# Kernel tuning notes

Measured on AMD Instinct MI355X. Metric: run time of the kernel, lower is better.

## Reference

```python
import jax, jax.numpy as jnp
import numpy as np
from functools import partial

SIGMA = 0.1       # blend_params.sigma (heaviside noise intensity)
GAMMA = 0.1       # blend_params.gamma (argmax noise intensity / z softening)
ZNEAR = 1.0
ZFAR = 100.0
NB_SAMPLES = 4
EPS = 1e-10
N, H, W, K = 8, 256, 256, 8


def random_heaviside(x, noise, sigma):
    # x: (N,H,W,K), noise: (S,N,H,W,K). torch.heaviside(v, ones): 1 for v>=0 else 0.
    maps = (x + sigma * noise >= 0).astype(x.dtype)
    return maps.mean(axis=0)


def random_argmax(z, noise, gamma):
    # z: (N,H,W,Kp), noise: (S,N,H,W,Kp). One-hot of per-sample argmax, averaged.
    zp = z + gamma * noise
    w = jax.nn.one_hot(jnp.argmax(zp, axis=-1), z.shape[-1], dtype=z.dtype)
    return w.mean(axis=0)


def reference(colors, dists, zbuf, pix_to_face, background):
    kh, ka = jax.random.split(jax.random.key(1))
    noise_h = jax.random.normal(kh, (NB_SAMPLES, N, H, W, K), dtype=colors.dtype)
    noise_a = jax.random.normal(ka, (NB_SAMPLES, N, H, W, K + 1), dtype=colors.dtype)

    mask = (pix_to_face >= 0).astype(colors.dtype)          # (N,H,W,K)
    prob_map = random_heaviside(-dists, noise_h, SIGMA) * mask
    alpha = jnp.prod(1.0 - prob_map, axis=-1)               # (N,H,W)

    z_inv = (ZFAR - zbuf) / (ZFAR - ZNEAR) * mask
    z_inv_max = jnp.clip(jnp.max(z_inv, axis=-1, keepdims=True), EPS)
    z_map = jnp.log(EPS + prob_map) + (z_inv - z_inv_max) / GAMMA
    bg_score = jnp.broadcast_to((EPS - z_inv_max) / GAMMA, z_map.shape[:-1] + (1,))
    z_map = jnp.concatenate([z_map, bg_score], axis=-1)     # (N,H,W,K+1)

    randomax = random_argmax(z_map, noise_a, GAMMA)
    wz, wb = randomax[..., :-1], randomax[..., -1:]
    weighted_colors = jnp.einsum('nhwk,nhwkc->nhwc', wz, colors)
    rgb = weighted_colors + wb * background                 # (N,H,W,3)
    a = (1.0 - alpha)[..., None]
    return jnp.concatenate([rgb, a], axis=-1)               # (N,H,W,4)


def setup_inputs() -> dict:
    key = jax.random.key(0)
    k1, k2, k3, k4 = jax.random.split(key, 4)
    colors = jax.random.normal(k1, (N, H, W, K, 3), dtype=jnp.float32)
    dists = jax.random.normal(k2, (N, H, W, K), dtype=jnp.float32)
    zbuf = jax.random.uniform(k3, (N, H, W, K), dtype=jnp.float32)
    pix_to_face = jax.random.randint(k4, (N, H, W, K), 0, 1000)
    background = jnp.ones((3,), dtype=jnp.float32)
    return {"colors": colors, "dists": dists, "zbuf": zbuf,
            "pix_to_face": pix_to_face, "background": background}
```

## Files before the change

kernel.cpp:

```cpp
#include <hip/hip_runtime.h>
#include <cstdint>
#include <cmath>


#pragma clang fp contract(off)

#define NPIX 524288
#define STRIDE_H 4194304u
#define STRIDE_A 4718592u
#define BAND_A 5e-5f
#define BAND_PACK 1.25e-4f
#define KEY_MASK 0xFFFFFFF0u
#define DET_THR 0.55f
#define ELIM_THR 1.10f

#define WAVE_FENCE() do {                                   \
    asm volatile("s_waitcnt lgkmcnt(0)" ::: "memory");      \
    __builtin_amdgcn_sched_barrier(0);                      \
  } while (0)

__device__ __forceinline__ uint32_t rotl32(uint32_t v, int n) {
  return (v << n) | (v >> (32 - n));
}

__device__ __forceinline__ void tf2x32(uint32_t k0, uint32_t k1,
                                       uint32_t c0, uint32_t c1,
                                       uint32_t& o0, uint32_t& o1) {
  const uint32_t k2 = k0 ^ k1 ^ 0x1BD11BDAu;
  uint32_t x0 = c0 + k0, x1 = c1 + k1;
#define TFR(r) { x0 += x1; x1 = rotl32(x1, r); x1 ^= x0; }
  TFR(13) TFR(15) TFR(26) TFR(6)
  x0 += k1;  x1 += k2 + 1u;
  TFR(17) TFR(29) TFR(16) TFR(24)
  x0 += k2;  x1 += k0 + 2u;
  TFR(13) TFR(15) TFR(26) TFR(6)
  x0 += k0;  x1 += k1 + 3u;
  TFR(17) TFR(29) TFR(16) TFR(24)
  x0 += k1;  x1 += k2 + 4u;
  TFR(13) TFR(15) TFR(26) TFR(6)
  x0 += k2;  x1 += k0 + 5u;
#undef TFR
  o0 = x0; o1 = x1;
}

__device__ __forceinline__ double fast_log(double z) {
  uint64_t b = __double_as_longlong(z);
  int E = (int)(b >> 52) - 1023;
  double m = __longlong_as_double((b & 0x000FFFFFFFFFFFFFULL) |
                                  0x3FF0000000000000ULL);
  bool c = m > 1.4142135623730951;
  m = c ? m * 0.5 : m;
  E = c ? E + 1 : E;
  double d = m + 1.0;
  double r = __builtin_amdgcn_rcp(d);
  r = fma(r, fma(-d, r, 1.0), r);
  r = fma(r, fma(-d, r, 1.0), r);
  double s = (m - 1.0) * r;
  double u = s * s;
  double p = 1.0 / 19.0;
  p = fma(p, u, 1.0 / 17.0);
  p = fma(p, u, 1.0 / 15.0);
  p = fma(p, u, 1.0 / 13.0);
  p = fma(p, u, 1.0 / 11.0);
  p = fma(p, u, 1.0 / 9.0);
  p = fma(p, u, 1.0 / 7.0);
  p = fma(p, u, 1.0 / 5.0);
  p = fma(p, u, 1.0 / 3.0);
  p = fma(p, u, 1.0);
  double lm = (2.0 * s) * p;
  const double LN2_HI = 6.93147180369123816490e-01;
  const double LN2_LO = 1.90821492927058770002e-10;
  double e = (double)E;
  return fma(e, LN2_HI, fma(e, LN2_LO, lm));
}

__device__ __forceinline__ float normal_exact(uint32_t bits) {
  float f = __uint_as_float((bits >> 9) | 0x3f800000u) - 1.0f;
  const float lo = __uint_as_float(0xBF7FFFFFu);
  float v = __fadd_rn(__fmul_rn(f, 2.0f), lo);
  v = fmaxf(lo, v);
  float t = -__fmul_rn(v, v);
  float taylor = __fmul_rn(__fadd_rn(__fmul_rn(-0.5f, t), 1.0f), t);
  float lg = (float)fast_log((double)__fadd_rn(t, 1.0f));
  float l1p = (fabsf(t) < 1e-4f) ? taylor : lg;
  float w = -l1p;
  const bool lt = w < 5.0f;
  float ww = lt ? __fsub_rn(w, 2.5f) : __fsub_rn(__fsqrt_rn(w), 3.0f);
  float p  = lt ? 2.81022636e-08f : -0.000200214257f;
  p = __fadd_rn(lt ?  3.43273939e-07f :  0.000100950558f, __fmul_rn(p, ww));
  p = __fadd_rn(lt ? -3.5233877e-06f  :  0.00134934322f,  __fmul_rn(p, ww));
  p = __fadd_rn(lt ? -4.39150654e-06f : -0.00367342844f,  __fmul_rn(p, ww));
  p = __fadd_rn(lt ?  0.00021858087f  :  0.00573950773f,  __fmul_rn(p, ww));
  p = __fadd_rn(lt ? -0.00125372503f  : -0.0076224613f,   __fmul_rn(p, ww));
  p = __fadd_rn(lt ? -0.00417768164f  :  0.00943887047f,  __fmul_rn(p, ww));
  p = __fadd_rn(lt ?  0.246640727f    :  1.00167406f,     __fmul_rn(p, ww));
  p = __fadd_rn(lt ?  1.50140941f     :  2.83297682f,     __fmul_rn(p, ww));
  return __fmul_rn(__uint_as_float(0x3FB504F3u), __fmul_rn(p, v));
}

__device__ __forceinline__ float score_fast(uint32_t bits, float zmj) {
  float f = __uint_as_float((bits >> 9) | 0x3f800000u) - 1.0f;
  const float lo = __uint_as_float(0xBF7FFFFFu);
  float v = fmaxf(lo, __fmaf_rn(f, 2.0f, lo));
  float t = -__fmul_rn(v, v);
  float u = __fadd_rn(t, 1.0f);
  float L = __builtin_amdgcn_logf(u);
  float ww = __fmaf_rn(-0.69314718f, L, -2.5f);
  float p = 2.81022636e-08f;
  p = __fmaf_rn(p, ww,  3.43273939e-07f);
  p = __fmaf_rn(p, ww, -3.5233877e-06f);
  p = __fmaf_rn(p, ww, -4.39150654e-06f);
  p = __fmaf_rn(p, ww,  0.00021858087f);
  p = __fmaf_rn(p, ww, -0.00125372503f);
  p = __fmaf_rn(p, ww, -0.00417768164f);
  p = __fmaf_rn(p, ww,  0.246640727f);
  p = __fmaf_rn(p, ww,  1.50140941f);
  if (__builtin_expect(__ballot(L <= -7.2134752f) != 0ull, 0)) {
    float w = __fmul_rn(-0.69314718f, L);
    float w2 = __builtin_amdgcn_sqrtf(w) - 3.0f;
    float q = -0.000200214257f;
    q = __fmaf_rn(q, w2,  0.000100950558f);
    q = __fmaf_rn(q, w2,  0.00134934322f);
    q = __fmaf_rn(q, w2, -0.00367342844f);
    q = __fmaf_rn(q, w2,  0.00573950773f);
    q = __fmaf_rn(q, w2, -0.0076224613f);
    q = __fmaf_rn(q, w2,  0.00943887047f);
    q = __fmaf_rn(q, w2,  1.00167406f);
    q = __fmaf_rn(q, w2,  2.83297682f);
    p = (L <= -7.2134752f) ? q : p;
  }
  return __fmaf_rn(__fmul_rn(p, v), 0.14142136f, zmj);
}

__device__ __forceinline__ uint32_t map_f32(float s) {
  uint32_t u = __float_as_uint(s);
  return u ^ ((uint32_t)((int32_t)u >> 31) | 0x80000000u);
}
__device__ __forceinline__ float unmap_f32(uint32_t m) {
  uint32_t u = m ^ ((uint32_t)((int32_t)(~m) >> 31) | 0x80000000u);
  return __uint_as_float(u);
}

__device__ __forceinline__ int thresh_m6(float d) {
  float y = fabsf(d) * 7.0710678f;
  float tt = __builtin_amdgcn_rcpf(__fmaf_rn(0.3275911f, y, 1.0f));
  float ex = __builtin_amdgcn_exp2f(__fmul_rn(-1.4426951f, y * y));
  float pp = 1.061405429f;
  pp = __fmaf_rn(pp, tt, -1.453152027f);
  pp = __fmaf_rn(pp, tt,  1.421413741f);
  pp = __fmaf_rn(pp, tt, -0.284496736f);
  pp = __fmaf_rn(pp, tt,  0.254829592f);
  float er = __fmaf_rn(-pp * tt, ex, 1.0f);
  float vs = copysignf(er, d);
  int T = (int)ceilf(__fmul_rn(__fadd_rn(vs, 0.99999994f), 4194304.0f));
  return T - 6;
}

__device__ __forceinline__ int wave_exscan4(int v, int& total) {
  int pre = 0; total = 0;
  #pragma unroll
  for (int b = 0; b < 4; ++b) {
    unsigned long long bl = __ballot(((v >> b) & 1) != 0);
    int below = (int)__builtin_amdgcn_mbcnt_hi(
        (uint32_t)(bl >> 32), __builtin_amdgcn_mbcnt_lo((uint32_t)bl, 0u));
    pre += below << b;
    total += (int)__popcll(bl) << b;
  }
  return pre;
}

__global__ __launch_bounds__(256) void RandomPhongShader_kernel(
    const float* __restrict__ colors,
    const float* __restrict__ dists,
    const float* __restrict__ zbuf,
    const int*   __restrict__ p2f,
    const float* __restrict__ bg,
    float* __restrict__ out)
{
  __shared__ float zmS[256][9];
  __shared__ __align__(8) unsigned char cntS[256][8];
  __shared__ unsigned short listS[4][576];
  __shared__ unsigned int s1S[4][64][4];
  __shared__ unsigned int s2S[4][64][4];

  const int tid  = threadIdx.x;
  const int lane = tid & 63;
  const int wv   = tid >> 6;
  const int P    = blockIdx.x * 256 + tid;
  const int Pw   = blockIdx.x * 256 + (wv << 6);

  uint32_t kh0, kh1, ka0, ka1;
  tf2x32(0u, 1u, 0u, 0u, kh0, kh1);
  tf2x32(0u, 1u, 0u, 1u, ka0, ka1);

  uint32_t ndm = 0, p4m = 0;
  {
    const float4* d4 = reinterpret_cast<const float4*>(dists + (size_t)P * 8);
    float4 a = d4[0], b = d4[1];
    float dk[8] = {a.x,a.y,a.z,a.w,b.x,b.y,b.z,b.w};
    #pragma unroll
    for (int k = 0; k < 8; ++k) {
      ndm |= (fabsf(dk[k]) < DET_THR) ? (1u << k) : 0u;
      p4m |= (dk[k] <= -DET_THR) ? (1u << k) : 0u;
    }
  }

  int Wtot;
  {
    int off = wave_exscan4(__builtin_popcount(ndm), Wtot);
    uint32_t m = ndm;
    int idx = off;
    while (m) {
      int k = __builtin_ctz(m); m &= m - 1;
      listS[wv][idx++] = (unsigned short)((lane << 3) | k);
    }
  }
  WAVE_FENCE();

  {
    const int trips = (Wtot + 63) >> 6;
    #pragma unroll 1
    for (int t = 0; t < trips; ++t) {
      const int i = (t << 6) + lane;
      const bool valid = i < Wtot;
      const unsigned short itm = listS[wv][valid ? i : 0];
      const int ow = itm >> 3, k = itm & 7;
      const int oTid = (wv << 6) | ow;
      const uint32_t base = (uint32_t)(Pw + ow) * 8u + (uint32_t)k;
      const float d = dists[(size_t)base];
      const int To = thresh_m6(d);
      uint32_t cnt = 0; bool band = false;
      #pragma unroll
      for (int s = 0; s < 4; ++s) {
        uint32_t o0, o1;
        tf2x32(kh0, kh1, 0u, base + (uint32_t)s * STRIDE_H, o0, o1);
        int mm = (int)((o0 ^ o1) >> 9);
        int sub = mm - To;
        cnt += (sub >= 6) ? 1u : 0u;
        band |= ((uint32_t)sub <= 12u);
      }
      if (__builtin_expect(__ballot(band && valid) != 0ull, 0)) {
        if (band && valid) {
          float x = -d;
          uint32_t c2 = 0;
          #pragma unroll 1
          for (int s = 0; s < 4; ++s) {
            uint32_t o0, o1;
            tf2x32(kh0, kh1, 0u, base + (uint32_t)s * STRIDE_H, o0, o1);
            float nz = normal_exact(o0 ^ o1);
            c2 += (__fadd_rn(x, __fmul_rn(0.1f, nz)) >= 0.0f) ? 1u : 0u;
          }
          cnt = c2;
        }
      }
      if (valid) cntS[oTid][k] = (unsigned char)cnt;
    }
  }
  WAVE_FENCE();

  uint32_t msk;
  {
    const int4* m4 = reinterpret_cast<const int4*>(p2f + (size_t)P * 8);
    int4 f = m4[0], g = m4[1];
    msk  = (f.x >= 0 ? 1u : 0u) | (f.y >= 0 ? 2u : 0u)
         | (f.z >= 0 ? 4u : 0u) | (f.w >= 0 ? 8u : 0u)
         | (g.x >= 0 ? 16u : 0u) | (g.y >= 0 ? 32u : 0u)
         | (g.z >= 0 ? 64u : 0u) | (g.w >= 0 ? 128u : 0u);
  }
  float zinv[8], zmax;
  {
    const float4* z4 = reinterpret_cast<const float4*>(zbuf + (size_t)P * 8);
    float4 c = z4[0], e = z4[1];
    float zk[8] = {c.x,c.y,c.z,c.w,e.x,e.y,e.z,e.w};
    #pragma unroll
    for (int k = 0; k < 8; ++k) {
      const float m = ((msk >> k) & 1u) ? 1.0f : 0.0f;
      float zi = __fmul_rn(__fdiv_rn(__fsub_rn(100.0f, zk[k]), 99.0f), m);
      zinv[k] = zi;
      zmax = (k == 0) ? zi : fmaxf(zmax, zi);
    }
  }
  zmax = fmaxf(zmax, 1e-10f);

  const float lg0 = (float)-23.025850916589025;
  const float lg1 = (float)-1.3862943611198906;
  const float lg2 = (float)-0.6931471805599453;
  const float lg3 = (float)-0.2876820724517809;

  const uint2 cg = *reinterpret_cast<const uint2*>(&cntS[tid][0]);
  float alpha = 1.0f;
  float zm[9];
  #pragma unroll
  for (int k = 0; k < 8; ++k) {
    const uint32_t byte_ = ((k < 4 ? cg.x : cg.y) >> (8 * (k & 3))) & 0xffu;
    const int cntk = ((ndm >> k) & 1u) ? (int)byte_
                    : ((((p4m >> k) & 1u) != 0u) ? 4 : 0);
    const bool mb = ((msk >> k) & 1u) != 0u;
    const float pm = mb ? __fmul_rn((float)cntk, 0.25f) : 0.0f;
    alpha *= (1.0f - pm);
    const int i = mb ? cntk : 0;
    const float lg = (i == 0) ? lg0 : (i == 1) ? lg1 : (i == 2) ? lg2
                   : (i == 3) ? lg3 : 0.0f;
    zm[k] = __fadd_rn(lg, __fdiv_rn(__fsub_rn(zinv[k], zmax), 0.1f));
    zmS[tid][k] = zm[k];
  }
  zm[8] = __fdiv_rn(__fsub_rn(1e-10f, zmax), 0.1f);
  zmS[tid][8] = zm[8];

  float bz = zm[0];
  #pragma unroll
  for (int j = 1; j < 9; ++j) bz = fmaxf(bz, zm[j]);
  const float thr = __fsub_rn(bz, ELIM_THR);
  uint32_t vm = 0;
  #pragma unroll
  for (int j = 0; j < 9; ++j) vm |= (zm[j] >= thr) ? (1u << j) : 0u;
  const int V  = __builtin_popcount(vm);
  const int j0 = __builtin_ctz(vm);

  int W3;
  {
    int off3 = wave_exscan4((V >= 2) ? V : 0, W3);
    uint32_t m = (V >= 2) ? vm : 0u;
    int idx = off3;
    while (m) {
      int j = __builtin_ctz(m); m &= m - 1;
      listS[wv][idx++] = (unsigned short)((lane << 4) | j);
    }
  }
  #pragma unroll
  for (int s = 0; s < 4; ++s) { s1S[wv][lane][s] = 0u; s2S[wv][lane][s] = 0u; }
  WAVE_FENCE();

  const int trips3 = (W3 + 63) >> 6;
  #pragma unroll 1
  for (int t = 0; t < trips3; ++t) {
    const int i = (t << 6) + lane;
    const bool valid = i < W3;
    const unsigned short itm = listS[wv][valid ? i : 0];
    const int ow = itm >> 4, j = itm & 15;
    const int oTid = (wv << 6) | ow;
    const float zo = zmS[oTid][j];
    const uint32_t cb3 = (uint32_t)(Pw + ow) * 9u + (uint32_t)j;
    const uint32_t jtag = (uint32_t)(15 - j);
    #pragma unroll
    for (int s = 0; s < 4; ++s) {
      uint32_t o0, o1;
      tf2x32(ka0, ka1, 0u, cb3 + (uint32_t)s * STRIDE_A, o0, o1);
      float sc = score_fast(o0 ^ o1, zo);
      uint32_t key = (map_f32(sc) & KEY_MASK) | jtag;
      if (valid) {
        uint32_t old = atomicMax(&s1S[wv][ow][s], key);
        uint32_t mn = key < old ? key : old;
        atomicMax(&s2S[wv][ow][s], mn);
      }
    }
  }
  WAVE_FENCE();

  uint32_t amPack = 0;
  const uint32_t cAo = (uint32_t)P * 9u;
  #pragma unroll 1
  for (int s = 0; s < 4; ++s) {
    int js;
    bool fl = false;
    if (V >= 2) {
      const uint32_t b1 = s1S[wv][lane][s];
      js = 15 - (int)(b1 & 0xFu);
      const float s1f = unmap_f32(b1 & KEY_MASK);
      const float s2f = unmap_f32(s2S[wv][lane][s] & KEY_MASK);
      fl = __fsub_rn(s1f, s2f) < BAND_PACK;
    } else {
      js = j0;
    }
    if (__builtin_expect(__ballot(fl) != 0ull, 0)) {
      if (fl) {
        int ame = 0;
        float be = -3.4e38f;
        #pragma unroll 1
        for (int j = 0; j < 9; ++j) {
          uint32_t o0, o1;
          tf2x32(ka0, ka1, 0u, cAo + (uint32_t)s * STRIDE_A + (uint32_t)j,
                 o0, o1);
          float nz = normal_exact(o0 ^ o1);
          float ve = __fadd_rn(zmS[tid][j], __fmul_rn(0.1f, nz));
          bool g = ve > be;
          be = g ? ve : be;
          ame = g ? j : ame;
        }
        js = ame;
      }
    }
    amPack += 1u << (3 * js);
  }

  float rgb[3] = {0.0f, 0.0f, 0.0f};
  {
    const float4* c4 = reinterpret_cast<const float4*>(colors + (size_t)P * 24);
    float cc[24];
    #pragma unroll
    for (int q = 0; q < 6; ++q) {
      float4 t = c4[q];
      cc[q*4+0]=t.x; cc[q*4+1]=t.y; cc[q*4+2]=t.z; cc[q*4+3]=t.w;
    }
    #pragma unroll
    for (int c = 0; c < 3; ++c) {
      float acc = 0.0f;
      #pragma unroll
      for (int k = 0; k < 8; ++k) {
        float wk = __fmul_rn(0.25f, (float)((amPack >> (3 * k)) & 7u));
        acc = __fadd_rn(acc, __fmul_rn(wk, cc[k * 3 + c]));
      }
      float wb = __fmul_rn(0.25f, (float)((amPack >> 24) & 7u));
      rgb[c] = __fadd_rn(acc, __fmul_rn(wb, bg[c]));
    }
  }

  float4 o;
  o.x = rgb[0]; o.y = rgb[1]; o.z = rgb[2];
  o.w = __fsub_rn(1.0f, alpha);
  reinterpret_cast<float4*>(out)[P] = o;
}

extern "C" void kernel_launch(void* const* d_in, const int* in_sizes, int n_in,
                              void* d_out, int out_size, void* d_ws, size_t ws_size,
                              hipStream_t stream) {
  const float* colors = (const float*)d_in[0];
  const float* dists  = (const float*)d_in[1];
  const float* zbuf   = (const float*)d_in[2];
  const int*   p2f    = (const int*)d_in[3];
  const float* bg     = (const float*)d_in[4];
  float* out = (float*)d_out;
  dim3 grid(NPIX / 256), block(256);
  hipLaunchKernelGGL(RandomPhongShader_kernel, grid, block, 0, stream,
                     colors, dists, zbuf, p2f, bg, out);
}
```

Before: 168.6 us.

## Hoist input loads, precompute thresholds, pack counts and flags in LDS

Loads of dists, p2f and zbuf are issued at kernel start, and the colors load is moved ahead of the argmax resolution so memory latency overlaps the RNG work. The per-item threshold is computed once per element and packed into the work list, so the heaviside loop no longer reloads dists except in the rare band-redo path. Counts are packed into one 3-bit-per-slot word with atomicOr, and the second-max array is replaced by a per-lane flag bitmask computed at atomicMax time. The per-wave lists share LDS through a union, lowering shared-memory use. In exchange, the coarser threshold band may send more elements down the exact redo path, and the extra atomics and register pressure from early loads could offset the gains.

```diff
diff --git a/kernel.cpp b/kernel.cpp
--- a/kernel.cpp
+++ b/kernel.cpp
@@ -13,6 +13,7 @@
 #define KEY_MASK 0xFFFFFFF0u
 #define DET_THR 0.55f
 #define ELIM_THR 1.10f
+#define HB_REDO 268
 
 #define WAVE_FENCE() do {                                   \
     asm volatile("s_waitcnt lgkmcnt(0)" ::: "memory");      \
@@ -178,10 +179,16 @@
     float* __restrict__ out)
 {
   __shared__ float zmS[256][9];
-  __shared__ __align__(8) unsigned char cntS[256][8];
-  __shared__ unsigned short listS[4][576];
-  __shared__ unsigned int s1S[4][64][4];
-  __shared__ unsigned int s2S[4][64][4];
+  __shared__ uint32_t cntP[256];
+  __shared__ uint32_t flagS[4][16];
+  union PerWave {
+    uint32_t hlist[512];
+    struct {
+      uint32_t s1[64][4];
+      unsigned short alist[576];
+    } p3;
+  };
+  __shared__ PerWave pwS[4];
 
   const int tid  = threadIdx.x;
   const int lane = tid & 63;
@@ -193,18 +200,21 @@
   tf2x32(0u, 1u, 0u, 0u, kh0, kh1);
   tf2x32(0u, 1u, 0u, 1u, ka0, ka1);
 
+  const float4* d4p = reinterpret_cast<const float4*>(dists + (size_t)P * 8);
+  const float4 da = d4p[0], db = d4p[1];
+  const int4* m4p = reinterpret_cast<const int4*>(p2f + (size_t)P * 8);
+  const int4 fa = m4p[0], fb = m4p[1];
+  const float4* z4p = reinterpret_cast<const float4*>(zbuf + (size_t)P * 8);
+  const float4 za = z4p[0], zb = z4p[1];
+
   uint32_t ndm = 0, p4m = 0;
-  {
-    const float4* d4 = reinterpret_cast<const float4*>(dists + (size_t)P * 8);
-    float4 a = d4[0], b = d4[1];
-    float dk[8] = {a.x,a.y,a.z,a.w,b.x,b.y,b.z,b.w};
-    #pragma unroll
-    for (int k = 0; k < 8; ++k) {
-      ndm |= (fabsf(dk[k]) < DET_THR) ? (1u << k) : 0u;
-      p4m |= (dk[k] <= -DET_THR) ? (1u << k) : 0u;
-    }
-  }
-
+  float dk[8] = {da.x,da.y,da.z,da.w,db.x,db.y,db.z,db.w};
+  #pragma unroll
+  for (int k = 0; k < 8; ++k) {
+    ndm |= (fabsf(dk[k]) < DET_THR) ? (1u << k) : 0u;
+    p4m |= (dk[k] <= -DET_THR) ? (1u << k) : 0u;
+  }
+  cntP[tid] = 0u;
   int Wtot;
   {
     int off = wave_exscan4(__builtin_popcount(ndm), Wtot);
@@ -212,9 +222,30 @@
     int idx = off;
     while (m) {
       int k = __builtin_ctz(m); m &= m - 1;
-      listS[wv][idx++] = (unsigned short)((lane << 3) | k);
-    }
-  }
+      int Tm6 = thresh_m6(dk[k]);
+      uint32_t Th = ((uint32_t)(Tm6 < 0 ? 0 : Tm6)) >> 8;
+      pwS[wv].hlist[idx++] = (Th << 9) | ((uint32_t)lane << 3) | (uint32_t)k;
+    }
+  }
+
+  uint32_t msk;
+  msk  = (fa.x >= 0 ? 1u : 0u) | (fa.y >= 0 ? 2u : 0u)
+       | (fa.z >= 0 ? 4u : 0u) | (fa.w >= 0 ? 8u : 0u)
+       | (fb.x >= 0 ? 16u : 0u) | (fb.y >= 0 ? 32u : 0u)
+       | (fb.z >= 0 ? 64u : 0u) | (fb.w >= 0 ? 128u : 0u);
+  float zinv[8], zmax;
+  {
+    float zk[8] = {za.x,za.y,za.z,za.w,zb.x,zb.y,zb.z,zb.w};
+    #pragma unroll
+    for (int k = 0; k < 8; ++k) {
+      const float m = ((msk >> k) & 1u) ? 1.0f : 0.0f;
+      float zi = __fmul_rn(__fdiv_rn(__fsub_rn(100.0f, zk[k]), 99.0f), m);
+      zinv[k] = zi;
+      zmax = (k == 0) ? zi : fmaxf(zmax, zi);
+    }
+  }
+  zmax = fmaxf(zmax, 1e-10f);
+
   WAVE_FENCE();
 
   {
@@ -223,25 +254,22 @@
     for (int t = 0; t < trips; ++t) {
       const int i = (t << 6) + lane;
       const bool valid = i < Wtot;
-      const unsigned short itm = listS[wv][valid ? i : 0];
-      const int ow = itm >> 3, k = itm & 7;
-      const int oTid = (wv << 6) | ow;
+      const uint32_t e = pwS[wv].hlist[valid ? i : 0];
+      const int ow = (int)((e >> 3) & 63u), k = (int)(e & 7u);
+      const uint32_t Th8 = (e >> 9) << 8;
       const uint32_t base = (uint32_t)(Pw + ow) * 8u + (uint32_t)k;
-      const float d = dists[(size_t)base];
-      const int To = thresh_m6(d);
       uint32_t cnt = 0; bool band = false;
       #pragma unroll
       for (int s = 0; s < 4; ++s) {
         uint32_t o0, o1;
         tf2x32(kh0, kh1, 0u, base + (uint32_t)s * STRIDE_H, o0, o1);
-        int mm = (int)((o0 ^ o1) >> 9);
-        int sub = mm - To;
-        cnt += (sub >= 6) ? 1u : 0u;
-        band |= ((uint32_t)sub <= 12u);
+        int sub8 = (int)((o0 ^ o1) >> 9) - (int)Th8;
+        cnt += (sub8 >= HB_REDO) ? 1u : 0u;
+        band |= ((uint32_t)sub8 < (uint32_t)HB_REDO);
       }
       if (__builtin_expect(__ballot(band && valid) != 0ull, 0)) {
         if (band && valid) {
-          float x = -d;
+          float x = -dists[(size_t)base];
           uint32_t c2 = 0;
           #pragma unroll 1
           for (int s = 0; s < 4; ++s) {
@@ -253,47 +281,23 @@
           cnt = c2;
         }
       }
-      if (valid) cntS[oTid][k] = (unsigned char)cnt;
+      if (valid) atomicOr(&cntP[(wv << 6) | ow], cnt << (3 * k));
     }
   }
   WAVE_FENCE();
 
-  uint32_t msk;
-  {
-    const int4* m4 = reinterpret_cast<const int4*>(p2f + (size_t)P * 8);
-    int4 f = m4[0], g = m4[1];
-    msk  = (f.x >= 0 ? 1u : 0u) | (f.y >= 0 ? 2u : 0u)
-         | (f.z >= 0 ? 4u : 0u) | (f.w >= 0 ? 8u : 0u)
-         | (g.x >= 0 ? 16u : 0u) | (g.y >= 0 ? 32u : 0u)
-         | (g.z >= 0 ? 64u : 0u) | (g.w >= 0 ? 128u : 0u);
-  }
-  float zinv[8], zmax;
-  {
-    const float4* z4 = reinterpret_cast<const float4*>(zbuf + (size_t)P * 8);
-    float4 c = z4[0], e = z4[1];
-    float zk[8] = {c.x,c.y,c.z,c.w,e.x,e.y,e.z,e.w};
-    #pragma unroll
-    for (int k = 0; k < 8; ++k) {
-      const float m = ((msk >> k) & 1u) ? 1.0f : 0.0f;
-      float zi = __fmul_rn(__fdiv_rn(__fsub_rn(100.0f, zk[k]), 99.0f), m);
-      zinv[k] = zi;
-      zmax = (k == 0) ? zi : fmaxf(zmax, zi);
-    }
-  }
-  zmax = fmaxf(zmax, 1e-10f);
+  const uint32_t cw = cntP[tid];
 
   const float lg0 = (float)-23.025850916589025;
   const float lg1 = (float)-1.3862943611198906;
   const float lg2 = (float)-0.6931471805599453;
   const float lg3 = (float)-0.2876820724517809;
 
-  const uint2 cg = *reinterpret_cast<const uint2*>(&cntS[tid][0]);
   float alpha = 1.0f;
   float zm[9];
   #pragma unroll
   for (int k = 0; k < 8; ++k) {
-    const uint32_t byte_ = ((k < 4 ? cg.x : cg.y) >> (8 * (k & 3))) & 0xffu;
-    const int cntk = ((ndm >> k) & 1u) ? (int)byte_
+    const int cntk = ((ndm >> k) & 1u) ? (int)((cw >> (3 * k)) & 7u)
                     : ((((p4m >> k) & 1u) != 0u) ? 4 : 0);
     const bool mb = ((msk >> k) & 1u) != 0u;
     const float pm = mb ? __fmul_rn((float)cntk, 0.25f) : 0.0f;
@@ -324,11 +328,12 @@
     int idx = off3;
     while (m) {
       int j = __builtin_ctz(m); m &= m - 1;
-      listS[wv][idx++] = (unsigned short)((lane << 4) | j);
-    }
-  }
-  #pragma unroll
-  for (int s = 0; s < 4; ++s) { s1S[wv][lane][s] = 0u; s2S[wv][lane][s] = 0u; }
+      pwS[wv].p3.alist[idx++] = (unsigned short)((lane << 4) | j);
+    }
+  }
+  #pragma unroll
+  for (int s = 0; s < 4; ++s) pwS[wv].p3.s1[lane][s] = 0u;
+  if (lane < 16) flagS[wv][lane] = 0u;
   WAVE_FENCE();
 
   const int trips3 = (W3 + 63) >> 6;
@@ -336,8 +341,8 @@
   for (int t = 0; t < trips3; ++t) {
     const int i = (t << 6) + lane;
     const bool valid = i < W3;
-    const unsigned short itm = listS[wv][valid ? i : 0];
-    const int ow = itm >> 4, j = itm & 15;
+    const unsigned short itm = pwS[wv].p3.alist[valid ? i : 0];
+    const int ow = (itm >> 4) & 63, j = itm & 15;
     const int oTid = (wv << 6) | ow;
     const float zo = zmS[oTid][j];
     const uint32_t cb3 = (uint32_t)(Pw + ow) * 9u + (uint32_t)j;
@@ -349,14 +354,28 @@
       float sc = score_fast(o0 ^ o1, zo);
       uint32_t key = (map_f32(sc) & KEY_MASK) | jtag;
       if (valid) {
-        uint32_t old = atomicMax(&s1S[wv][ow][s], key);
-        uint32_t mn = key < old ? key : old;
-        atomicMax(&s2S[wv][ow][s], mn);
+        uint32_t old = atomicMax(&pwS[wv].p3.s1[ow][s], key);
+        uint32_t hi = key > old ? key : old;
+        uint32_t lo2 = key > old ? old : key;
+        float d12 = __fsub_rn(unmap_f32(hi & KEY_MASK), unmap_f32(lo2 & KEY_MASK));
+        if (d12 < BAND_PACK)
+          atomicOr(&flagS[wv][ow >> 2], 1u << (((ow & 3) << 2) + s));
       }
     }
   }
   WAVE_FENCE();
 
+  float cc[24];
+  {
+    const float4* c4 = reinterpret_cast<const float4*>(colors + (size_t)P * 24);
+    #pragma unroll
+    for (int q = 0; q < 6; ++q) {
+      float4 t = c4[q];
+      cc[q*4+0]=t.x; cc[q*4+1]=t.y; cc[q*4+2]=t.z; cc[q*4+3]=t.w;
+    }
+  }
+
+  const uint32_t flagw = flagS[wv][lane >> 2];
   uint32_t amPack = 0;
   const uint32_t cAo = (uint32_t)P * 9u;
   #pragma unroll 1
@@ -364,11 +383,9 @@
     int js;
     bool fl = false;
     if (V >= 2) {
-      const uint32_t b1 = s1S[wv][lane][s];
+      const uint32_t b1 = pwS[wv].p3.s1[lane][s];
       js = 15 - (int)(b1 & 0xFu);
-      const float s1f = unmap_f32(b1 & KEY_MASK);
-      const float s2f = unmap_f32(s2S[wv][lane][s] & KEY_MASK);
-      fl = __fsub_rn(s1f, s2f) < BAND_PACK;
+      fl = ((flagw >> (((lane & 3) << 2) + s)) & 1u) != 0u;
     } else {
       js = j0;
     }
@@ -393,26 +410,17 @@
     amPack += 1u << (3 * js);
   }
 
-  float rgb[3] = {0.0f, 0.0f, 0.0f};
-  {
-    const float4* c4 = reinterpret_cast<const float4*>(colors + (size_t)P * 24);
-    float cc[24];
+  float rgb[3];
+  #pragma unroll
+  for (int c = 0; c < 3; ++c) {
+    float acc = 0.0f;
     #pragma unroll
-    for (int q = 0; q < 6; ++q) {
-      float4 t = c4[q];
-      cc[q*4+0]=t.x; cc[q*4+1]=t.y; cc[q*4+2]=t.z; cc[q*4+3]=t.w;
-    }
-    #pragma unroll
-    for (int c = 0; c < 3; ++c) {
-      float acc = 0.0f;
-      #pragma unroll
-      for (int k = 0; k < 8; ++k) {
-        float wk = __fmul_rn(0.25f, (float)((amPack >> (3 * k)) & 7u));
-        acc = __fadd_rn(acc, __fmul_rn(wk, cc[k * 3 + c]));
-      }
-      float wb = __fmul_rn(0.25f, (float)((amPack >> 24) & 7u));
-      rgb[c] = __fadd_rn(acc, __fmul_rn(wb, bg[c]));
-    }
+    for (int k = 0; k < 8; ++k) {
+      float wk = __fmul_rn(0.25f, (float)((amPack >> (3 * k)) & 7u));
+      acc = __fadd_rn(acc, __fmul_rn(wk, cc[k * 3 + c]));
+    }
+    float wb = __fmul_rn(0.25f, (float)((amPack >> 24) & 7u));
+    rgb[c] = __fadd_rn(acc, __fmul_rn(wb, bg[c]));
   }
 
   float4 o;
```

New measurement: 177.7 us. 1.05x slower.

## Hoist global loads early, prefetch next-trip dists, transpose shared atomic arrays

Applied to the files above, without the earlier changes.

Issues the dists, pix_to_face and zbuf loads together at kernel start and computes the mask and z_inv before the first wave fence, so their latency overlaps the list-building work. The heaviside loop software-prefetches the next trip's list entry and dists value. The per-sample max arrays are transposed to [s][lane] with padding, and the sample order is rotated by lane, to reduce LDS bank conflicts in the atomics. Colors are loaded before the argmax resolution loop so that latency is hidden. This raises register pressure, which may lower occupancy.

```diff
diff --git a/kernel.cpp b/kernel.cpp
--- a/kernel.cpp
+++ b/kernel.cpp
@@ -180,8 +180,8 @@
   __shared__ float zmS[256][9];
   __shared__ __align__(8) unsigned char cntS[256][8];
   __shared__ unsigned short listS[4][576];
-  __shared__ unsigned int s1S[4][64][4];
-  __shared__ unsigned int s2S[4][64][4];
+  __shared__ unsigned int s1S[4][4][66];
+  __shared__ unsigned int s2S[4][4][66];
 
   const int tid  = threadIdx.x;
   const int lane = tid & 63;
@@ -193,11 +193,16 @@
   tf2x32(0u, 1u, 0u, 0u, kh0, kh1);
   tf2x32(0u, 1u, 0u, 1u, ka0, ka1);
 
+  const float4* d4p = reinterpret_cast<const float4*>(dists + (size_t)P * 8);
+  const float4 da = d4p[0], db = d4p[1];
+  const int4* m4p = reinterpret_cast<const int4*>(p2f + (size_t)P * 8);
+  const int4 fa = m4p[0], fb = m4p[1];
+  const float4* z4p = reinterpret_cast<const float4*>(zbuf + (size_t)P * 8);
+  const float4 za = z4p[0], zb = z4p[1];
+
   uint32_t ndm = 0, p4m = 0;
   {
-    const float4* d4 = reinterpret_cast<const float4*>(dists + (size_t)P * 8);
-    float4 a = d4[0], b = d4[1];
-    float dk[8] = {a.x,a.y,a.z,a.w,b.x,b.y,b.z,b.w};
+    float dk[8] = {da.x,da.y,da.z,da.w,db.x,db.y,db.z,db.w};
     #pragma unroll
     for (int k = 0; k < 8; ++k) {
       ndm |= (fabsf(dk[k]) < DET_THR) ? (1u << k) : 0u;
@@ -215,19 +220,53 @@
       listS[wv][idx++] = (unsigned short)((lane << 3) | k);
     }
   }
+
+  uint32_t msk;
+  msk  = (fa.x >= 0 ? 1u : 0u) | (fa.y >= 0 ? 2u : 0u)
+       | (fa.z >= 0 ? 4u : 0u) | (fa.w >= 0 ? 8u : 0u)
+       | (fb.x >= 0 ? 16u : 0u) | (fb.y >= 0 ? 32u : 0u)
+       | (fb.z >= 0 ? 64u : 0u) | (fb.w >= 0 ? 128u : 0u);
+  float zinv[8], zmax;
+  {
+    float zk[8] = {za.x,za.y,za.z,za.w,zb.x,zb.y,zb.z,zb.w};
+    #pragma unroll
+    for (int k = 0; k < 8; ++k) {
+      const float m = ((msk >> k) & 1u) ? 1.0f : 0.0f;
+      float zi = __fmul_rn(__fdiv_rn(__fsub_rn(100.0f, zk[k]), 99.0f), m);
+      zinv[k] = zi;
+      zmax = (k == 0) ? zi : fmaxf(zmax, zi);
+    }
+  }
+  zmax = fmaxf(zmax, 1e-10f);
+
   WAVE_FENCE();
 
   {
     const int trips = (Wtot + 63) >> 6;
+    unsigned short itmN = 0; float dN = 0.0f;
+    if (trips > 0) {
+      const bool v0 = lane < Wtot;
+      itmN = listS[wv][v0 ? lane : 0];
+      const uint32_t bN =
+          (uint32_t)(Pw + ((itmN >> 3) & 63)) * 8u + (uint32_t)(itmN & 7u);
+      dN = dists[(size_t)bN];
+    }
     #pragma unroll 1
     for (int t = 0; t < trips; ++t) {
-      const int i = (t << 6) + lane;
-      const bool valid = i < Wtot;
-      const unsigned short itm = listS[wv][valid ? i : 0];
-      const int ow = itm >> 3, k = itm & 7;
+      const unsigned short itm = itmN;
+      const float d = dN;
+      const bool valid = (t << 6) + lane < Wtot;
+      if (t + 1 < trips) {
+        const int i2 = ((t + 1) << 6) + lane;
+        const bool v2 = i2 < Wtot;
+        itmN = listS[wv][v2 ? i2 : 0];
+        const uint32_t bN =
+            (uint32_t)(Pw + ((itmN >> 3) & 63)) * 8u + (uint32_t)(itmN & 7u);
+        dN = dists[(size_t)bN];
+      }
+      const int ow = (itm >> 3) & 63, k = itm & 7;
       const int oTid = (wv << 6) | ow;
       const uint32_t base = (uint32_t)(Pw + ow) * 8u + (uint32_t)k;
-      const float d = dists[(size_t)base];
       const int To = thresh_m6(d);
       uint32_t cnt = 0; bool band = false;
       #pragma unroll
@@ -258,30 +297,6 @@
   }
   WAVE_FENCE();
 
-  uint32_t msk;
-  {
-    const int4* m4 = reinterpret_cast<const int4*>(p2f + (size_t)P * 8);
-    int4 f = m4[0], g = m4[1];
-    msk  = (f.x >= 0 ? 1u : 0u) | (f.y >= 0 ? 2u : 0u)
-         | (f.z >= 0 ? 4u : 0u) | (f.w >= 0 ? 8u : 0u)
-         | (g.x >= 0 ? 16u : 0u) | (g.y >= 0 ? 32u : 0u)
-         | (g.z >= 0 ? 64u : 0u) | (g.w >= 0 ? 128u : 0u);
-  }
-  float zinv[8], zmax;
-  {
-    const float4* z4 = reinterpret_cast<const float4*>(zbuf + (size_t)P * 8);
-    float4 c = z4[0], e = z4[1];
-    float zk[8] = {c.x,c.y,c.z,c.w,e.x,e.y,e.z,e.w};
-    #pragma unroll
-    for (int k = 0; k < 8; ++k) {
-      const float m = ((msk >> k) & 1u) ? 1.0f : 0.0f;
-      float zi = __fmul_rn(__fdiv_rn(__fsub_rn(100.0f, zk[k]), 99.0f), m);
-      zinv[k] = zi;
-      zmax = (k == 0) ? zi : fmaxf(zmax, zi);
-    }
-  }
-  zmax = fmaxf(zmax, 1e-10f);
-
   const float lg0 = (float)-23.025850916589025;
   const float lg1 = (float)-1.3862943611198906;
   const float lg2 = (float)-0.6931471805599453;
@@ -328,7 +343,7 @@
     }
   }
   #pragma unroll
-  for (int s = 0; s < 4; ++s) { s1S[wv][lane][s] = 0u; s2S[wv][lane][s] = 0u; }
+  for (int s = 0; s < 4; ++s) { s1S[wv][s][lane] = 0u; s2S[wv][s][lane] = 0u; }
   WAVE_FENCE();
 
   const int trips3 = (W3 + 63) >> 6;
@@ -337,25 +352,36 @@
     const int i = (t << 6) + lane;
     const bool valid = i < W3;
     const unsigned short itm = listS[wv][valid ? i : 0];
-    const int ow = itm >> 4, j = itm & 15;
+    const int ow = (itm >> 4) & 63, j = itm & 15;
     const int oTid = (wv << 6) | ow;
     const float zo = zmS[oTid][j];
     const uint32_t cb3 = (uint32_t)(Pw + ow) * 9u + (uint32_t)j;
     const uint32_t jtag = (uint32_t)(15 - j);
     #pragma unroll
-    for (int s = 0; s < 4; ++s) {
+    for (int sq = 0; sq < 4; ++sq) {
+      const int s = (sq + lane) & 3;
       uint32_t o0, o1;
       tf2x32(ka0, ka1, 0u, cb3 + (uint32_t)s * STRIDE_A, o0, o1);
       float sc = score_fast(o0 ^ o1, zo);
       uint32_t key = (map_f32(sc) & KEY_MASK) | jtag;
       if (valid) {
-        uint32_t old = atomicMax(&s1S[wv][ow][s], key);
+        uint32_t old = atomicMax(&s1S[wv][s][ow], key);
         uint32_t mn = key < old ? key : old;
-        atomicMax(&s2S[wv][ow][s], mn);
+        atomicMax(&s2S[wv][s][ow], mn);
       }
     }
   }
   WAVE_FENCE();
+
+  float cc[24];
+  {
+    const float4* c4 = reinterpret_cast<const float4*>(colors + (size_t)P * 24);
+    #pragma unroll
+    for (int q = 0; q < 6; ++q) {
+      float4 t = c4[q];
+      cc[q*4+0]=t.x; cc[q*4+1]=t.y; cc[q*4+2]=t.z; cc[q*4+3]=t.w;
+    }
+  }
 
   uint32_t amPack = 0;
   const uint32_t cAo = (uint32_t)P * 9u;
@@ -364,10 +390,10 @@
     int js;
     bool fl = false;
     if (V >= 2) {
-      const uint32_t b1 = s1S[wv][lane][s];
+      const uint32_t b1 = s1S[wv][s][lane];
       js = 15 - (int)(b1 & 0xFu);
       const float s1f = unmap_f32(b1 & KEY_MASK);
-      const float s2f = unmap_f32(s2S[wv][lane][s] & KEY_MASK);
+      const float s2f = unmap_f32(s2S[wv][s][lane] & KEY_MASK);
       fl = __fsub_rn(s1f, s2f) < BAND_PACK;
     } else {
       js = j0;
@@ -393,26 +419,17 @@
     amPack += 1u << (3 * js);
   }
 
-  float rgb[3] = {0.0f, 0.0f, 0.0f};
-  {
-    const float4* c4 = reinterpret_cast<const float4*>(colors + (size_t)P * 24);
-    float cc[24];
+  float rgb[3];
+  #pragma unroll
+  for (int c = 0; c < 3; ++c) {
+    float acc = 0.0f;
     #pragma unroll
-    for (int q = 0; q < 6; ++q) {
-      float4 t = c4[q];
-      cc[q*4+0]=t.x; cc[q*4+1]=t.y; cc[q*4+2]=t.z; cc[q*4+3]=t.w;
-    }
-    #pragma unroll
-    for (int c = 0; c < 3; ++c) {
-      float acc = 0.0f;
-      #pragma unroll
-      for (int k = 0; k < 8; ++k) {
-        float wk = __fmul_rn(0.25f, (float)((amPack >> (3 * k)) & 7u));
-        acc = __fadd_rn(acc, __fmul_rn(wk, cc[k * 3 + c]));
-      }
-      float wb = __fmul_rn(0.25f, (float)((amPack >> 24) & 7u));
-      rgb[c] = __fadd_rn(acc, __fmul_rn(wb, bg[c]));
-    }
+    for (int k = 0; k < 8; ++k) {
+      float wk = __fmul_rn(0.25f, (float)((amPack >> (3 * k)) & 7u));
+      acc = __fadd_rn(acc, __fmul_rn(wk, cc[k * 3 + c]));
+    }
+    float wb = __fmul_rn(0.25f, (float)((amPack >> 24) & 7u));
+    rgb[c] = __fadd_rn(acc, __fmul_rn(wb, bg[c]));
   }
 
   float4 o;
```

Result: no change. 171.0 us (+1.4%).
